# Kernel tuning notes

Hardware: AMD Instinct MI355X
Metric: run time of the kernel (lower is better)

Reference implementation:

```python
import jax, jax.numpy as jnp
import numpy as np

NEG_SLOPE_GAT = 0.2   # GATConv internal leaky_relu slope (PyG default)
NEG_SLOPE = 0.01      # nn.LeakyReLU default slope


def _gat(h_src_in, h_dst_in, src, dst, Wsrc, Wdst, a_s, a_d, b, n_dst, self_loops):
    """Single-head PyG-style GATConv: gather -> score -> edge softmax -> scatter-sum."""
    hs = h_src_in @ Wsrc            # [N_src, C]
    hd = h_dst_in @ Wdst            # [N_dst, C]
    if self_loops:                  # static flag; same node set on both sides
        loop = jnp.arange(n_dst, dtype=src.dtype)
        src = jnp.concatenate([src, loop])
        dst = jnp.concatenate([dst, loop])
    # attention logits per edge
    e = jax.nn.leaky_relu((hs @ a_s)[src] + (hd @ a_d)[dst], NEG_SLOPE_GAT)  # [E]
    # softmax over edges sharing a destination node
    m = jax.ops.segment_max(e, dst, num_segments=n_dst)
    ex = jnp.exp(e - m[dst])
    denom = jax.ops.segment_sum(ex, dst, num_segments=n_dst)
    alpha = ex / denom[dst]
    out = jax.ops.segment_sum(hs[src] * alpha[:, None], dst, num_segments=n_dst)
    return out + b


def setup_inputs() -> dict:
    key = jax.random.key(0)
    ks = iter(jax.random.split(key, 64))
    NB, NP = 100_000, 50_000
    E_bb, E_pp, E_bp = 800_000, 400_000, 400_000
    FB, FP, H, H2 = 32, 34, 64, 32
    rn = lambda shape, s=0.05: jax.random.normal(next(ks), shape, jnp.float32) * s
    d = {}
    d['x_b'] = rn((NB, FB), 1.0)
    d['x_p'] = rn((NP, FP), 1.0)
    d['ei_bb'] = jax.random.randint(next(ks), (2, E_bb), 0, NB, jnp.int32)
    d['ei_pp'] = jax.random.randint(next(ks), (2, E_pp), 0, NP, jnp.int32)
    d['ei_bp_src'] = jax.random.randint(next(ks), (E_bp,), 0, NB, jnp.int32)
    d['ei_bp_dst'] = jax.random.randint(next(ks), (E_bp,), 0, NP, jnp.int32)
    d['W_in_b'] = rn((FB, H)); d['b_in_b'] = jnp.zeros((H,), jnp.float32)
    d['W_in_p'] = rn((FP, H)); d['b_in_p'] = jnp.zeros((H,), jnp.float32)
    for tag, cin, cout in (('1', H, H), ('2', H, H2)):
        d['W_bb' + tag] = rn((cin, cout)); d['as_bb' + tag] = rn((cout,)); d['ad_bb' + tag] = rn((cout,)); d['b_bb' + tag] = jnp.zeros((cout,), jnp.float32)
        d['W_pp' + tag] = rn((cin, cout)); d['as_pp' + tag] = rn((cout,)); d['ad_pp' + tag] = rn((cout,)); d['b_pp' + tag] = jnp.zeros((cout,), jnp.float32)
        d['Ws_bp' + tag] = rn((cin, cout)); d['Wd_bp' + tag] = rn((cin, cout)); d['as_bp' + tag] = rn((cout,)); d['ad_bp' + tag] = rn((cout,)); d['b_bp' + tag] = jnp.zeros((cout,), jnp.float32)
    d['W_out'] = rn((H2, 1)); d['b_out'] = jnp.zeros((1,), jnp.float32)
    return d


def reference(x_b, x_p, ei_bb, ei_pp, ei_bp_src, ei_bp_dst,
              W_in_b, b_in_b, W_in_p, b_in_p,
              W_bb1, as_bb1, ad_bb1, b_bb1, W_pp1, as_pp1, ad_pp1, b_pp1,
              Ws_bp1, Wd_bp1, as_bp1, ad_bp1, b_bp1,
              W_bb2, as_bb2, ad_bb2, b_bb2, W_pp2, as_pp2, ad_pp2, b_pp2,
              Ws_bp2, Wd_bp2, as_bp2, ad_bp2, b_bp2,
              W_out, b_out):
    NB, NP = x_b.shape[0], x_p.shape[0]
    lr = lambda v: jax.nn.leaky_relu(v, NEG_SLOPE)
    # input projections (dropout is eval-mode identity)
    hb = lr(x_b @ W_in_b + b_in_b)
    hp = lr(x_p @ W_in_p + b_in_p)
    # hetero conv 1 (sum aggregation over relations sharing a dst type)
    ob = _gat(hb, hb, ei_bb[0], ei_bb[1], W_bb1, W_bb1, as_bb1, ad_bb1, b_bb1, NB, True)
    op = (_gat(hp, hp, ei_pp[0], ei_pp[1], W_pp1, W_pp1, as_pp1, ad_pp1, b_pp1, NP, True)
          + _gat(hb, hp, ei_bp_src, ei_bp_dst, Ws_bp1, Wd_bp1, as_bp1, ad_bp1, b_bp1, NP, False))
    hb, hp = lr(ob), lr(op)
    # hetero conv 2
    ob2 = _gat(hb, hb, ei_bb[0], ei_bb[1], W_bb2, W_bb2, as_bb2, ad_bb2, b_bb2, NB, True)
    op2 = (_gat(hp, hp, ei_pp[0], ei_pp[1], W_pp2, W_pp2, as_pp2, ad_pp2, b_pp2, NP, True)
           + _gat(hb, hp, ei_bp_src, ei_bp_dst, Ws_bp2, Wd_bp2, as_bp2, ad_bp2, b_bp2, NP, False))
    hp = lr(op2)
    return hp @ W_out + b_out  # [NP, 1]
```

## Files before the change

kernel.cpp:

```cpp
#include <hip/hip_runtime.h>
#include <hip/hip_bf16.h>
#include <cstdint>
#include <cstddef>


typedef __attribute__((ext_vector_type(8))) short short8;
typedef __attribute__((ext_vector_type(4))) float f32x4;
typedef unsigned int u32;

#define ABITS 9
#define CHUNKE 4096

static __device__ __forceinline__ float b2f(__hip_bfloat16 v) { return __bfloat162float(v); }

static __device__ __forceinline__ float ldf(const void* p, int i, int bf) {
    return bf ? __bfloat162float(((const __hip_bfloat16*)p)[i]) : ((const float*)p)[i];
}

static __device__ __forceinline__ short f2bs(float f) {
    __hip_bfloat16 h = __float2bfloat16(f);
    return *reinterpret_cast<short*>(&h);
}
static __device__ __forceinline__ float bs2f(short s) {
    __hip_bfloat16 h = *reinterpret_cast<__hip_bfloat16*>(&s);
    return __bfloat162float(h);
}
static __device__ __forceinline__ float lo16(u32 u) { return bs2f((short)(u & 0xffffu)); }
static __device__ __forceinline__ float hi16(u32 u) { return bs2f((short)(u >> 16)); }
static __device__ __forceinline__ u32 pack2(float x, float y) {
    return (u32)(unsigned short)f2bs(x) | ((u32)(unsigned short)f2bs(y) << 16);
}
static __device__ __forceinline__ float sel4(const float* a, int i) {
    return i == 0 ? a[0] : i == 1 ? a[1] : i == 2 ? a[2] : a[3];
}
static __device__ __forceinline__ float lrelu2(float x) { return x > 0.f ? x : 0.2f * x; }

__global__ __launch_bounds__(256) void k_detect(const unsigned* __restrict__ w,
                                                int* __restrict__ flag)
{
    __shared__ int s_cnt;
    if (threadIdx.x == 0) s_cnt = 0;
    __syncthreads();
    int c = 0;
#pragma unroll
    for (int j = 0; j < 4; ++j) {
        unsigned u = w[threadIdx.x * 4 + j];
        unsigned e = (u >> 7) & 0xffu;
        c += (e >= 100u && e <= 145u) ? 1 : 0;
    }
    atomicAdd(&s_cnt, c);
    __syncthreads();
    if (threadIdx.x == 0) *flag = (s_cnt > 614) ? 1 : 0;
}

__global__ __launch_bounds__(256) void k_bkt_hist(
    const int* __restrict__ bb_d, const int* __restrict__ pp_d,
    const int* __restrict__ bp_d, int* __restrict__ histM,
    int E_bb, int E_pp, int E_bp, int NB, int NP, int nbkt, int nblk)
{
    __shared__ int h[512];
    for (int i = threadIdx.x; i < nbkt; i += 256) h[i] = 0;
    __syncthreads();
    int E_all = E_bb + E_pp + E_bp;
    int base = blockIdx.x * CHUNKE;
    int end = base + CHUNKE < E_all ? base + CHUNKE : E_all;
    for (int i = base + threadIdx.x; i < end; i += 256) {
        int d;
        if (i < E_bb) d = bb_d[i];
        else if (i < E_bb + E_pp) d = NB + pp_d[i - E_bb];
        else d = NB + NP + bp_d[i - E_bb - E_pp];
        atomicAdd(&h[d >> ABITS], 1);
    }
    __syncthreads();
    for (int i = threadIdx.x; i < nbkt; i += 256)
        histM[(size_t)i * nblk + blockIdx.x] = h[i];
}

__global__ __launch_bounds__(1024) void k_scan1(const int* __restrict__ deg,
                                                int* __restrict__ out,
                                                int* __restrict__ bsum, int n)
{
    __shared__ int wsum[16];
    int gid = blockIdx.x * 1024 + threadIdx.x;
    int lane = threadIdx.x & 63, wid = threadIdx.x >> 6;
    int v = (gid < n) ? deg[gid] : 0;
    int x = v;
#pragma unroll
    for (int off = 1; off < 64; off <<= 1) {
        int y = __shfl_up(x, off, 64);
        if (lane >= off) x += y;
    }
    if (lane == 63) wsum[wid] = x;
    __syncthreads();
    if (wid == 0 && lane < 16) {
        int w0 = wsum[lane];
#pragma unroll
        for (int off = 1; off < 16; off <<= 1) {
            int y = __shfl_up(w0, off, 16);
            if (lane >= off) w0 += y;
        }
        wsum[lane] = w0;
    }
    __syncthreads();
    int base = (wid > 0) ? wsum[wid - 1] : 0;
    int incl = base + x;
    if (gid < n) out[gid] = incl - v;
    if (threadIdx.x == 1023) bsum[blockIdx.x] = incl;
}

__global__ __launch_bounds__(1024) void k_scan2(int* __restrict__ bsum, int nb)
{
    __shared__ int wsum[16];
    int lane = threadIdx.x & 63, wid = threadIdx.x >> 6;
    int v = (threadIdx.x < nb) ? bsum[threadIdx.x] : 0;
    int x = v;
#pragma unroll
    for (int off = 1; off < 64; off <<= 1) {
        int y = __shfl_up(x, off, 64);
        if (lane >= off) x += y;
    }
    if (lane == 63) wsum[wid] = x;
    __syncthreads();
    if (wid == 0 && lane < 16) {
        int w0 = wsum[lane];
#pragma unroll
        for (int off = 1; off < 16; off <<= 1) {
            int y = __shfl_up(w0, off, 16);
            if (lane >= off) w0 += y;
        }
        wsum[lane] = w0;
    }
    __syncthreads();
    int base = (wid > 0) ? wsum[wid - 1] : 0;
    if (threadIdx.x < nb) bsum[threadIdx.x] = base + x - v;
}

__global__ __launch_bounds__(1024) void k_scan3(int* __restrict__ indptr,
                                                const int* __restrict__ bsum,
                                                int n, int E)
{
    int gid = blockIdx.x * 1024 + threadIdx.x;
    if (gid < n) indptr[gid] += bsum[blockIdx.x];
    if (gid == 0) indptr[n] = E;
}

__global__ __launch_bounds__(256) void k_bkt_scatter(
    const int* __restrict__ bb_s, const int* __restrict__ bb_d,
    const int* __restrict__ pp_s, const int* __restrict__ pp_d,
    const int* __restrict__ bp_s, const int* __restrict__ bp_d,
    const int* __restrict__ histS, unsigned* __restrict__ ebuf,
    int E_bb, int E_pp, int E_bp, int NB, int NP, int nbkt, int nblk)
{
    __shared__ int cur[512];
    for (int i = threadIdx.x; i < nbkt; i += 256)
        cur[i] = histS[(size_t)i * nblk + blockIdx.x];
    __syncthreads();
    int E_all = E_bb + E_pp + E_bp;
    int base = blockIdx.x * CHUNKE;
    int end = base + CHUNKE < E_all ? base + CHUNKE : E_all;
    for (int i = base + threadIdx.x; i < end; i += 256) {
        int s, d;
        if (i < E_bb) { s = bb_s[i]; d = bb_d[i]; }
        else if (i < E_bb + E_pp) { int j = i - E_bb; s = pp_s[j]; d = NB + pp_d[j]; }
        else { int j = i - E_bb - E_pp; s = bp_s[j]; d = NB + NP + bp_d[j]; }
        int p = atomicAdd(&cur[d >> ABITS], 1);
        ebuf[p] = ((unsigned)(d & ((1 << ABITS) - 1)) << 20) | (unsigned)s;
    }
}

__global__ __launch_bounds__(256) void k_deg(
    const unsigned* __restrict__ ebuf, const int* __restrict__ histS,
    int* __restrict__ deg, int NALL, int E_all, int nbkt, int nblk)
{
    __shared__ int h[1 << ABITS];
    int b = blockIdx.x;
    int d0 = b << ABITS;
    int nloc = NALL - d0 < (1 << ABITS) ? NALL - d0 : (1 << ABITS);
    for (int i = threadIdx.x; i < nloc; i += 256) h[i] = 0;
    __syncthreads();
    int s0 = histS[(size_t)b * nblk];
    int s1 = histS[(size_t)(b + 1) * nblk];
    for (int i = s0 + threadIdx.x; i < s1; i += 256)
        atomicAdd(&h[ebuf[i] >> 20], 1);
    __syncthreads();
    for (int i = threadIdx.x; i < nloc; i += 256) deg[d0 + i] = h[i];
}

__global__ __launch_bounds__(256) void k_place(
    const unsigned* __restrict__ ebuf, const int* __restrict__ histS,
    const int* __restrict__ ip, int* __restrict__ sidx,
    int NALL, int E_all, int nbkt, int nblk)
{
    __shared__ int cur[1 << ABITS];
    int b = blockIdx.x;
    int d0 = b << ABITS;
    int nloc = NALL - d0 < (1 << ABITS) ? NALL - d0 : (1 << ABITS);
    for (int i = threadIdx.x; i < nloc; i += 256) cur[i] = ip[d0 + i];
    __syncthreads();
    int s0 = histS[(size_t)b * nblk];
    int s1 = histS[(size_t)(b + 1) * nblk];
    for (int i = s0 + threadIdx.x; i < s1; i += 256) {
        unsigned e = ebuf[i];
        int p = atomicAdd(&cur[e >> 20], 1);
        sidx[p] = (int)(e & 0xFFFFFu);
    }
}

template <int CIN>
__global__ __launch_bounds__(256) void k_in_proj_mfma(
    const void* __restrict__ X, const void* __restrict__ W, const void* __restrict__ B,
    __hip_bfloat16* __restrict__ Y, int M, const int* __restrict__ flag)
{
    const int bf = *flag;
    constexpr int KP = 40;
    __shared__ short WT[64 * KP];
    __shared__ float bl[64];
    for (int i = threadIdx.x; i < 64 * CIN; i += 256) {
        int n = i / CIN, k = i - n * CIN;
        WT[n * KP + k] = f2bs(ldf(W, k * 64 + n, bf));
    }
    if (threadIdx.x < 64) bl[threadIdx.x] = ldf(B, threadIdx.x, bf);
    __syncthreads();

    int lane = threadIdx.x & 63;
    int wv   = threadIdx.x >> 6;
    int m = lane & 15, quad = lane >> 4;
    int row0 = (blockIdx.x * 4 + wv) * 16;
    if (row0 >= M) return;

    int arow = row0 + m; if (arow >= M) arow = M - 1;
    short8 a;
#pragma unroll
    for (int j = 0; j < 8; ++j)
        a[j] = f2bs(ldf(X, arow * CIN + quad * 8 + j, bf));

    f32x4 acc[4] = {};
#pragma unroll
    for (int t = 0; t < 4; ++t) {
        short8 b = *(const short8*)&WT[((lane & 15) + 16 * t) * KP + quad * 8];
        acc[t] = __builtin_amdgcn_mfma_f32_16x16x32_bf16(a, b, acc[t], 0, 0, 0);
    }

    if (CIN == 34) {
        float x32[4], x33[4];
#pragma unroll
        for (int r = 0; r < 4; ++r) {
            int row = row0 + quad * 4 + r; if (row >= M) row = M - 1;
            x32[r] = ldf(X, row * CIN + 32, bf);
            x33[r] = ldf(X, row * CIN + 33, bf);
        }
#pragma unroll
        for (int t = 0; t < 4; ++t) {
            int col = (lane & 15) + 16 * t;
            float w32 = bs2f(WT[col * KP + 32]);
            float w33 = bs2f(WT[col * KP + 33]);
#pragma unroll
            for (int r = 0; r < 4; ++r)
                acc[t][r] += x32[r] * w32 + x33[r] * w33;
        }
    }

#pragma unroll
    for (int t = 0; t < 4; ++t) {
        int col = (lane & 15) + 16 * t;
        float bb = bl[col];
#pragma unroll
        for (int r = 0; r < 4; ++r) {
            int row = row0 + quad * 4 + r;
            if (row < M) {
                float v = acc[t][r] + bb;
                v = v > 0.f ? v : 0.01f * v;
                Y[(size_t)row * 64 + col] = __float2bfloat16(v);
            }
        }
    }
}

template <int N, bool STORE>
__global__ __launch_bounds__(256) void k_gat_proj_mfma(
    const __hip_bfloat16* __restrict__ H, const void* __restrict__ W,
    const void* __restrict__ a_s, const void* __restrict__ a_d,
    __hip_bfloat16* __restrict__ HS, float* __restrict__ SS, float* __restrict__ SD,
    int M, const int* __restrict__ flag)
{
    const int bf = *flag;
    constexpr int KP = 72;
    constexpr int T = N / 16;
    __shared__ short WT[N * KP];
    for (int i = threadIdx.x; i < N * 64; i += 256) {
        int n = i >> 6, k = i & 63;
        WT[n * KP + k] = f2bs(ldf(W, k * N + n, bf));
    }
    __syncthreads();

    int lane = threadIdx.x & 63;
    int wv   = threadIdx.x >> 6;
    int m = lane & 15, quad = lane >> 4;
    int row0 = (blockIdx.x * 4 + wv) * 16;
    if (row0 >= M) return;

    const short* Hs = (const short*)H;
    int arow = row0 + m; if (arow >= M) arow = M - 1;

    f32x4 acc[T] = {};
#pragma unroll
    for (int ks = 0; ks < 2; ++ks) {
        short8 a = *(const short8*)&Hs[(size_t)arow * 64 + ks * 32 + quad * 8];
#pragma unroll
        for (int t = 0; t < T; ++t) {
            short8 b = *(const short8*)&WT[((lane & 15) + 16 * t) * KP + ks * 32 + quad * 8];
            acc[t] = __builtin_amdgcn_mfma_f32_16x16x32_bf16(a, b, acc[t], 0, 0, 0);
        }
    }

    float asv[T], adv[T];
#pragma unroll
    for (int t = 0; t < T; ++t) {
        int col = (lane & 15) + 16 * t;
        asv[t] = ldf(a_s, col, bf);
        adv[t] = ldf(a_d, col, bf);
    }
    float vs[4] = {}, vd[4] = {};
#pragma unroll
    for (int t = 0; t < T; ++t)
#pragma unroll
        for (int r = 0; r < 4; ++r) {
            vs[r] += acc[t][r] * asv[t];
            vd[r] += acc[t][r] * adv[t];
        }
#pragma unroll
    for (int off = 1; off < 16; off <<= 1)
#pragma unroll
        for (int r = 0; r < 4; ++r) {
            vs[r] += __shfl_xor(vs[r], off);
            vd[r] += __shfl_xor(vd[r], off);
        }
    int c = lane & 15;
    if (c < 8) {
        int row = row0 + quad * 4 + (c & 3);
        if (row < M) {
            if (c < 4) SS[row] = sel4(vs, c & 3);
            else       SD[row] = sel4(vd, c & 3);
        }
    }

    if (STORE) {
#pragma unroll
        for (int t = 0; t < T; ++t) {
            int col = (lane & 15) + 16 * t;
#pragma unroll
            for (int r = 0; r < 4; ++r) {
                int row = row0 + quad * 4 + r;
                if (row < M)
                    HS[(size_t)row * N + col] = __float2bfloat16(acc[t][r]);
            }
        }
    }
}

template <int N1, int N2, bool S1, bool S2>
__global__ __launch_bounds__(256) void k_gat_proj_dual(
    const __hip_bfloat16* __restrict__ H,
    const void* __restrict__ W1, const void* __restrict__ W2,
    const void* __restrict__ as1, const void* __restrict__ ad1,
    const void* __restrict__ as2, const void* __restrict__ ad2,
    __hip_bfloat16* __restrict__ HS1, __hip_bfloat16* __restrict__ HS2,
    float* __restrict__ SS1, float* __restrict__ SD1,
    float* __restrict__ SS2, float* __restrict__ SD2,
    int M, const int* __restrict__ flag)
{
    const int bf = *flag;
    constexpr int KP = 72;
    constexpr int T1 = N1 / 16, T2 = N2 / 16, T = T1 + T2;
    __shared__ short WT[(N1 + N2) * KP];
    for (int i = threadIdx.x; i < N1 * 64; i += 256) {
        int n = i >> 6, k = i & 63;
        WT[n * KP + k] = f2bs(ldf(W1, k * N1 + n, bf));
    }
    for (int i = threadIdx.x; i < N2 * 64; i += 256) {
        int n = i >> 6, k = i & 63;
        WT[(N1 + n) * KP + k] = f2bs(ldf(W2, k * N2 + n, bf));
    }
    __syncthreads();

    int lane = threadIdx.x & 63;
    int wv   = threadIdx.x >> 6;
    int m = lane & 15, quad = lane >> 4;
    int row0 = (blockIdx.x * 4 + wv) * 16;
    if (row0 >= M) return;

    const short* Hs = (const short*)H;
    int arow = row0 + m; if (arow >= M) arow = M - 1;

    f32x4 acc[T] = {};
#pragma unroll
    for (int ks = 0; ks < 2; ++ks) {
        short8 a = *(const short8*)&Hs[(size_t)arow * 64 + ks * 32 + quad * 8];
#pragma unroll
        for (int t = 0; t < T; ++t) {
            short8 b = *(const short8*)&WT[((lane & 15) + 16 * t) * KP + ks * 32 + quad * 8];
            acc[t] = __builtin_amdgcn_mfma_f32_16x16x32_bf16(a, b, acc[t], 0, 0, 0);
        }
    }

    float vs1[4] = {}, vd1[4] = {}, vs2[4] = {}, vd2[4] = {};
#pragma unroll
    for (int t = 0; t < T1; ++t) {
        int col = (lane & 15) + 16 * t;
        float av = ldf(as1, col, bf), dv = ldf(ad1, col, bf);
#pragma unroll
        for (int r = 0; r < 4; ++r) {
            vs1[r] += acc[t][r] * av;
            vd1[r] += acc[t][r] * dv;
        }
    }
#pragma unroll
    for (int t = 0; t < T2; ++t) {
        int col = (lane & 15) + 16 * t;
        float av = ldf(as2, col, bf), dv = ldf(ad2, col, bf);
#pragma unroll
        for (int r = 0; r < 4; ++r) {
            vs2[r] += acc[T1 + t][r] * av;
            vd2[r] += acc[T1 + t][r] * dv;
        }
    }
#pragma unroll
    for (int off = 1; off < 16; off <<= 1)
#pragma unroll
        for (int r = 0; r < 4; ++r) {
            vs1[r] += __shfl_xor(vs1[r], off);
            vd1[r] += __shfl_xor(vd1[r], off);
            vs2[r] += __shfl_xor(vs2[r], off);
            vd2[r] += __shfl_xor(vd2[r], off);
        }
    int c = lane & 15;
    {
        int row = row0 + quad * 4 + (c & 3);
        if (row < M) {
            if (c < 4)       SS1[row] = sel4(vs1, c & 3);
            else if (c < 8)  SD1[row] = sel4(vd1, c & 3);
            else if (c < 12) SS2[row] = sel4(vs2, c & 3);
            else             SD2[row] = sel4(vd2, c & 3);
        }
    }

    if (S1) {
#pragma unroll
        for (int t = 0; t < T1; ++t) {
            int col = (lane & 15) + 16 * t;
#pragma unroll
            for (int r = 0; r < 4; ++r) {
                int row = row0 + quad * 4 + r;
                if (row < M)
                    HS1[(size_t)row * N1 + col] = __float2bfloat16(acc[t][r]);
            }
        }
    }
    if (S2) {
#pragma unroll
        for (int t = 0; t < T2; ++t) {
            int col = (lane & 15) + 16 * t;
#pragma unroll
            for (int r = 0; r < 4; ++r) {
                int row = row0 + quad * 4 + r;
                if (row < M)
                    HS2[(size_t)row * N2 + col] = __float2bfloat16(acc[T1 + t][r]);
            }
        }
    }
}

__global__ __launch_bounds__(256) void k_gather1(
    const int* __restrict__ ip, const int* __restrict__ si,
    const float* __restrict__ SS, const float* __restrict__ SD,
    const __hip_bfloat16* __restrict__ HS, const void* __restrict__ bias,
    __hip_bfloat16* __restrict__ OUT, int M, const int* __restrict__ flag)
{
    const int bf = *flag;
    int lane = threadIdx.x & 63;
    int half = lane >> 5, hl = lane & 31;
    int d = blockIdx.x * 4 + (threadIdx.x >> 6);
    if (d >= M) return;
    const u32* H32 = (const u32*)HS;
    float sdd = SD[d];
    float ax = 0.f, ay = 0.f, den = 0.f;
    if (half == 0) {
        float ex = __expf(lrelu2(SS[d] + sdd));
        u32 h = H32[(size_t)d * 32 + hl];
        ax = lo16(h) * ex; ay = hi16(h) * ex; den = ex;
    }
    int j1 = ip[d + 1];
    int j = ip[d] + half;
    for (; j + 2 < j1; j += 4) {
        int s0 = si[j], s1 = si[j + 2];
        u32 h0 = H32[(size_t)s0 * 32 + hl];
        u32 h1 = H32[(size_t)s1 * 32 + hl];
        float e0 = __expf(lrelu2(SS[s0] + sdd));
        float e1 = __expf(lrelu2(SS[s1] + sdd));
        ax += lo16(h0) * e0 + lo16(h1) * e1;
        ay += hi16(h0) * e0 + hi16(h1) * e1;
        den += e0 + e1;
    }
    if (j < j1) {
        int s0 = si[j];
        u32 h0 = H32[(size_t)s0 * 32 + hl];
        float e0 = __expf(lrelu2(SS[s0] + sdd));
        ax += lo16(h0) * e0; ay += hi16(h0) * e0; den += e0;
    }
    ax += __shfl_xor(ax, 32); ay += __shfl_xor(ay, 32); den += __shfl_xor(den, 32);
    if (half == 0) {
        float vx = ax / den + ldf(bias, 2 * hl, bf);
        float vy = ay / den + ldf(bias, 2 * hl + 1, bf);
        vx = vx > 0.f ? vx : 0.01f * vx;
        vy = vy > 0.f ? vy : 0.01f * vy;
        ((u32*)OUT)[(size_t)d * 32 + hl] = pack2(vx, vy);
    }
}

__global__ __launch_bounds__(256) void k_gather2(
    const int* __restrict__ ip1, const int* __restrict__ si,
    const float* __restrict__ SS1, const float* __restrict__ SD1,
    const __hip_bfloat16* __restrict__ HS1,
    const int* __restrict__ ip2,
    const float* __restrict__ SS2, const float* __restrict__ SD2,
    const __hip_bfloat16* __restrict__ HS2,
    const void* __restrict__ b1, const void* __restrict__ b2,
    __hip_bfloat16* __restrict__ OUT, int M, const int* __restrict__ flag)
{
    const int bf = *flag;
    int lane = threadIdx.x & 63;
    int half = lane >> 5, hl = lane & 31;
    int d = blockIdx.x * 4 + (threadIdx.x >> 6);
    if (d >= M) return;
    const u32* H1 = (const u32*)HS1;
    const u32* H2 = (const u32*)HS2;
    float sdd = SD1[d];
    float a1x = 0.f, a1y = 0.f, den1 = 0.f;
    if (half == 0) {
        float ex = __expf(lrelu2(SS1[d] + sdd));
        u32 h = H1[(size_t)d * 32 + hl];
        a1x = lo16(h) * ex; a1y = hi16(h) * ex; den1 = ex;
    }
    int j1 = ip1[d + 1];
    int j = ip1[d] + half;
    for (; j + 2 < j1; j += 4) {
        int s0 = si[j], s1 = si[j + 2];
        u32 h0 = H1[(size_t)s0 * 32 + hl];
        u32 h1 = H1[(size_t)s1 * 32 + hl];
        float e0 = __expf(lrelu2(SS1[s0] + sdd));
        float e1 = __expf(lrelu2(SS1[s1] + sdd));
        a1x += lo16(h0) * e0 + lo16(h1) * e1;
        a1y += hi16(h0) * e0 + hi16(h1) * e1;
        den1 += e0 + e1;
    }
    if (j < j1) {
        int s0 = si[j];
        u32 h0 = H1[(size_t)s0 * 32 + hl];
        float e0 = __expf(lrelu2(SS1[s0] + sdd));
        a1x += lo16(h0) * e0; a1y += hi16(h0) * e0; den1 += e0;
    }
    float sdd2 = SD2[d];
    float a2x = 0.f, a2y = 0.f, den2 = 0.f;
    j1 = ip2[d + 1];
    j = ip2[d] + half;
    for (; j + 2 < j1; j += 4) {
        int s0 = si[j], s1 = si[j + 2];
        u32 h0 = H2[(size_t)s0 * 32 + hl];
        u32 h1 = H2[(size_t)s1 * 32 + hl];
        float e0 = __expf(lrelu2(SS2[s0] + sdd2));
        float e1 = __expf(lrelu2(SS2[s1] + sdd2));
        a2x += lo16(h0) * e0 + lo16(h1) * e1;
        a2y += hi16(h0) * e0 + hi16(h1) * e1;
        den2 += e0 + e1;
    }
    if (j < j1) {
        int s0 = si[j];
        u32 h0 = H2[(size_t)s0 * 32 + hl];
        float e0 = __expf(lrelu2(SS2[s0] + sdd2));
        a2x += lo16(h0) * e0; a2y += hi16(h0) * e0; den2 += e0;
    }
    a1x += __shfl_xor(a1x, 32); a1y += __shfl_xor(a1y, 32); den1 += __shfl_xor(den1, 32);
    a2x += __shfl_xor(a2x, 32); a2y += __shfl_xor(a2y, 32); den2 += __shfl_xor(den2, 32);
    if (half == 0) {
        float inv2 = den2 > 0.f ? 1.f / den2 : 0.f;
        float vx = a1x / den1 + a2x * inv2 + ldf(b1, 2 * hl, bf) + ldf(b2, 2 * hl, bf);
        float vy = a1y / den1 + a2y * inv2 + ldf(b1, 2 * hl + 1, bf) + ldf(b2, 2 * hl + 1, bf);
        vx = vx > 0.f ? vx : 0.01f * vx;
        vy = vy > 0.f ? vy : 0.01f * vy;
        ((u32*)OUT)[(size_t)d * 32 + hl] = pack2(vx, vy);
    }
}

__global__ __launch_bounds__(256) void k_gather_out(
    const int* __restrict__ ip1, const int* __restrict__ si,
    const float* __restrict__ SS1, const float* __restrict__ SD1,
    const __hip_bfloat16* __restrict__ HS1,
    const int* __restrict__ ip2,
    const float* __restrict__ SS2, const float* __restrict__ SD2,
    const __hip_bfloat16* __restrict__ HS2,
    const void* __restrict__ b1, const void* __restrict__ b2,
    const void* __restrict__ Wout, const void* __restrict__ bout,
    void* __restrict__ OUT, int M, const int* __restrict__ flag)
{
    const int bf = *flag;
    int lane = threadIdx.x & 63;
    int q = lane >> 4, hl = lane & 15;
    int d = blockIdx.x * 4 + (threadIdx.x >> 6);
    if (d >= M) return;
    const u32* H1 = (const u32*)HS1;
    const u32* H2 = (const u32*)HS2;
    float sdd = SD1[d];
    float a1x = 0.f, a1y = 0.f, den1 = 0.f;
    if (q == 0) {
        float ex = __expf(lrelu2(SS1[d] + sdd));
        u32 h = H1[(size_t)d * 16 + hl];
        a1x = lo16(h) * ex; a1y = hi16(h) * ex; den1 = ex;
    }
    int j1 = ip1[d + 1];
    for (int j = ip1[d] + q; j < j1; j += 4) {
        int s0 = si[j];
        u32 h0 = H1[(size_t)s0 * 16 + hl];
        float e0 = __expf(lrelu2(SS1[s0] + sdd));
        a1x += lo16(h0) * e0; a1y += hi16(h0) * e0; den1 += e0;
    }
    float sdd2 = SD2[d];
    float a2x = 0.f, a2y = 0.f, den2 = 0.f;
    j1 = ip2[d + 1];
    for (int j = ip2[d] + q; j < j1; j += 4) {
        int s0 = si[j];
        u32 h0 = H2[(size_t)s0 * 16 + hl];
        float e0 = __expf(lrelu2(SS2[s0] + sdd2));
        a2x += lo16(h0) * e0; a2y += hi16(h0) * e0; den2 += e0;
    }
    a1x += __shfl_xor(a1x, 16); a1y += __shfl_xor(a1y, 16); den1 += __shfl_xor(den1, 16);
    a2x += __shfl_xor(a2x, 16); a2y += __shfl_xor(a2y, 16); den2 += __shfl_xor(den2, 16);
    a1x += __shfl_xor(a1x, 32); a1y += __shfl_xor(a1y, 32); den1 += __shfl_xor(den1, 32);
    a2x += __shfl_xor(a2x, 32); a2y += __shfl_xor(a2y, 32); den2 += __shfl_xor(den2, 32);
    float inv2 = den2 > 0.f ? 1.f / den2 : 0.f;
    float vx = a1x / den1 + a2x * inv2 + ldf(b1, 2 * hl, bf) + ldf(b2, 2 * hl, bf);
    float vy = a1y / den1 + a2y * inv2 + ldf(b1, 2 * hl + 1, bf) + ldf(b2, 2 * hl + 1, bf);
    vx = vx > 0.f ? vx : 0.01f * vx;
    vy = vy > 0.f ? vy : 0.01f * vy;
    float t = vx * ldf(Wout, 2 * hl, bf) + vy * ldf(Wout, 2 * hl + 1, bf);
#pragma unroll
    for (int off = 1; off < 16; off <<= 1) t += __shfl_xor(t, off);
    if (lane == 0) {
        float r = t + ldf(bout, 0, bf);
        if (bf) ((__hip_bfloat16*)OUT)[d] = __float2bfloat16(r);
        else    ((float*)OUT)[d] = r;
    }
}

extern "C" void kernel_launch(void* const* d_in, const int* in_sizes, int n_in,
                              void* d_out, int out_size, void* d_ws, size_t ws_size,
                              hipStream_t stream)
{
    const void* x_b = d_in[0];
    const void* x_p = d_in[1];
    const int* ei_bb = (const int*)d_in[2];
    const int* ei_pp = (const int*)d_in[3];
    const int* bp_s  = (const int*)d_in[4];
    const int* bp_d  = (const int*)d_in[5];
    const void *W_in_b = d_in[6],  *b_in_b = d_in[7];
    const void *W_in_p = d_in[8],  *b_in_p = d_in[9];
    const void *W_bb1 = d_in[10], *as_bb1 = d_in[11], *ad_bb1 = d_in[12], *b_bb1 = d_in[13];
    const void *W_pp1 = d_in[14], *as_pp1 = d_in[15], *ad_pp1 = d_in[16], *b_pp1 = d_in[17];
    const void *Ws_bp1 = d_in[18], *Wd_bp1 = d_in[19], *as_bp1 = d_in[20], *ad_bp1 = d_in[21], *b_bp1 = d_in[22];
    const void *W_pp2 = d_in[27], *as_pp2 = d_in[28], *ad_pp2 = d_in[29], *b_pp2 = d_in[30];
    const void *Ws_bp2 = d_in[31], *Wd_bp2 = d_in[32], *as_bp2 = d_in[33], *ad_bp2 = d_in[34], *b_bp2 = d_in[35];
    const void *W_out = d_in[36], *b_out = d_in[37];

    const int NB   = in_sizes[0] / 32;
    const int NP   = in_sizes[1] / 34;
    const int E_bb = in_sizes[2] / 2;
    const int E_pp = in_sizes[3] / 2;
    const int E_bp = in_sizes[4];
    const int E_all = E_bb + E_pp + E_bp;
    const int NALL  = NB + 2 * NP;
    const int* bb_s = ei_bb;  const int* bb_d = ei_bb + E_bb;
    const int* pp_s = ei_pp;  const int* pp_d = ei_pp + E_pp;
    (void)ws_size; (void)n_in; (void)out_size;

    const int nbkt  = (NALL + (1 << ABITS) - 1) >> ABITS;
    const int nblk  = (E_all + CHUNKE - 1) / CHUNKE;
    const int nh    = nbkt * nblk;

    typedef __hip_bfloat16 bf16;
    char* base = (char*)d_ws;
    size_t o = 0;
    auto alloc = [&](size_t bytes) { char* p = base + o; o += (bytes + 255) & ~(size_t)255; return p; };

    int* flag  = (int*)alloc(256);
    int* bsum  = (int*)alloc(1024 * 4);
    int* histM = (int*)alloc((size_t)nh * 4);
    int* histS = (int*)alloc((size_t)(nh + 1) * 4);
    int* degA  = (int*)alloc((size_t)NALL * 4);
    int* ip_all = (int*)alloc((size_t)(NALL + 1) * 4);
    unsigned* ebuf = (unsigned*)alloc((size_t)E_all * 4);
    int* si_all = (int*)alloc((size_t)E_all * 4);
    float* ss_bb = (float*)alloc((size_t)NB * 4);
    float* sd_bb = (float*)alloc((size_t)NB * 4);
    float* ss_bp = (float*)alloc((size_t)NB * 4);
    float* ss_pp = (float*)alloc((size_t)NP * 4);
    float* sd_pp = (float*)alloc((size_t)NP * 4);
    float* sd_bp = (float*)alloc((size_t)NP * 4);
    float* ss2_bp = ss_bb;
    float* ss2_pp = ss_pp;
    float* sd2_pp = sd_pp;
    float* sd2_bp = sd_bp;
    float* junkNB = (float*)degA;
    float* junkNP = (float*)(degA + NB);

    char* S1 = alloc((size_t)NB * 64 * 2);
    char* S2 = alloc((size_t)NP * 64 * 2);
    char* S3 = alloc((size_t)NB * 64 * 2);
    char* S4 = alloc((size_t)NB * 64 * 2);
    char* S5 = alloc((size_t)NB * 64 * 2);
    char* S6 = alloc((size_t)NP * 64 * 2);

    bf16* hb     = (bf16*)S1;
    bf16* hp     = (bf16*)S2;
    bf16* hs_bb  = (bf16*)S3;
    bf16* hb2    = (bf16*)S4;
    bf16* hs_bp  = (bf16*)S5;
    bf16* hs_pp  = (bf16*)S6;
    bf16* hp2    = (bf16*)S3;
    bf16* hs2_pp = (bf16*)S2;
    bf16* hs2_bp = (bf16*)S1;

    auto cdiv = [](int a, int b) { return (a + b - 1) / b; };

    k_detect<<<1, 256, 0, stream>>>((const unsigned*)x_b, flag);

    k_bkt_hist<<<nblk, 256, 0, stream>>>(bb_d, pp_d, bp_d, histM,
                                         E_bb, E_pp, E_bp, NB, NP, nbkt, nblk);
    int sb1 = cdiv(nh, 1024);
    k_scan1<<<sb1, 1024, 0, stream>>>(histM, histS, bsum, nh);
    k_scan2<<<1, 1024, 0, stream>>>(bsum, sb1);
    k_scan3<<<sb1, 1024, 0, stream>>>(histS, bsum, nh, E_all);
    k_bkt_scatter<<<nblk, 256, 0, stream>>>(bb_s, bb_d, pp_s, pp_d, bp_s, bp_d,
                                            histS, ebuf, E_bb, E_pp, E_bp, NB, NP, nbkt, nblk);
    k_deg<<<nbkt, 256, 0, stream>>>(ebuf, histS, degA, NALL, E_all, nbkt, nblk);
    int sb2 = cdiv(NALL, 1024);
    k_scan1<<<sb2, 1024, 0, stream>>>(degA, ip_all, bsum, NALL);
    k_scan2<<<1, 1024, 0, stream>>>(bsum, sb2);
    k_scan3<<<sb2, 1024, 0, stream>>>(ip_all, bsum, NALL, E_all);
    k_place<<<nbkt, 256, 0, stream>>>(ebuf, histS, ip_all, si_all, NALL, E_all, nbkt, nblk);

    const int* ip_bb = ip_all;
    const int* ip_pp = ip_all + NB;
    const int* ip_bp = ip_all + NB + NP;

    k_in_proj_mfma<32><<<cdiv(NB, 64), 256, 0, stream>>>(x_b, W_in_b, b_in_b, hb, NB, flag);
    k_in_proj_mfma<34><<<cdiv(NP, 64), 256, 0, stream>>>(x_p, W_in_p, b_in_p, hp, NP, flag);

    k_gat_proj_dual<64, 64, true, true><<<cdiv(NB, 64), 256, 0, stream>>>(
        hb, W_bb1, Ws_bp1, as_bb1, ad_bb1, as_bp1, ad_bp1,
        hs_bb, hs_bp, ss_bb, sd_bb, ss_bp, junkNB, NB, flag);
    k_gather1<<<cdiv(NB, 4), 256, 0, stream>>>(ip_bb, si_all, ss_bb, sd_bb, hs_bb, b_bb1, hb2, NB, flag);

    k_gat_proj_dual<64, 64, true, false><<<cdiv(NP, 64), 256, 0, stream>>>(
        hp, W_pp1, Wd_bp1, as_pp1, ad_pp1, as_bp1, ad_bp1,
        hs_pp, nullptr, ss_pp, sd_pp, junkNP, sd_bp, NP, flag);
    k_gather2<<<cdiv(NP, 4), 256, 0, stream>>>(ip_pp, si_all, ss_pp, sd_pp, hs_pp,
                                               ip_bp, ss_bp, sd_bp, hs_bp,
                                               b_pp1, b_bp1, hp2, NP, flag);

    k_gat_proj_dual<32, 32, true, false><<<cdiv(NP, 64), 256, 0, stream>>>(
        hp2, W_pp2, Wd_bp2, as_pp2, ad_pp2, as_bp2, ad_bp2,
        hs2_pp, nullptr, ss2_pp, sd2_pp, junkNP, sd2_bp, NP, flag);
    k_gat_proj_mfma<32, true><<<cdiv(NB, 64), 256, 0, stream>>>(
        hb2, Ws_bp2, as_bp2, ad_bp2, hs2_bp, ss2_bp, junkNB, NB, flag);

    k_gather_out<<<cdiv(NP, 4), 256, 0, stream>>>(ip_pp, si_all, ss2_pp, sd2_pp, hs2_pp,
                                                  ip_bp, ss2_bp, sd2_bp, hs2_bp,
                                                  b_pp2, b_bp2, W_out, b_out, d_out, NP, flag);
}
```

Measured before the change: 434.1 us.

## Merge CSR build passes and fuse paired projection/gather launches

Folds the dtype detection into the histogram kernel. Replaces the degree count, three-pass scan and placement kernels with one per-bucket finalize kernel that does a local scan using the bucket offsets. Merges the B/P input projections, the layer-1 projections, the layer-1 gathers and the layer-2 projections into single launches that dispatch on block index. The aim is to cut kernel launch and serialization overhead; buffers are re-aliased to free the degree array.

```diff
diff --git a/kernel.cpp b/kernel.cpp
--- a/kernel.cpp
+++ b/kernel.cpp
@@ -7,22 +7,23 @@
 typedef __attribute__((ext_vector_type(8))) short short8;
 typedef __attribute__((ext_vector_type(4))) float f32x4;
 typedef unsigned int u32;
+typedef __hip_bfloat16 bf16;
 
 #define ABITS 9
 #define CHUNKE 4096
 
-static __device__ __forceinline__ float b2f(__hip_bfloat16 v) { return __bfloat162float(v); }
+static __device__ __forceinline__ float b2f(bf16 v) { return __bfloat162float(v); }
 
 static __device__ __forceinline__ float ldf(const void* p, int i, int bf) {
-    return bf ? __bfloat162float(((const __hip_bfloat16*)p)[i]) : ((const float*)p)[i];
+    return bf ? __bfloat162float(((const bf16*)p)[i]) : ((const float*)p)[i];
 }
 
 static __device__ __forceinline__ short f2bs(float f) {
-    __hip_bfloat16 h = __float2bfloat16(f);
+    bf16 h = __float2bfloat16(f);
     return *reinterpret_cast<short*>(&h);
 }
 static __device__ __forceinline__ float bs2f(short s) {
-    __hip_bfloat16 h = *reinterpret_cast<__hip_bfloat16*>(&s);
+    bf16 h = *reinterpret_cast<bf16*>(&s);
     return __bfloat162float(h);
 }
 static __device__ __forceinline__ float lo16(u32 u) { return bs2f((short)(u & 0xffffu)); }
@@ -35,30 +36,28 @@
 }
 static __device__ __forceinline__ float lrelu2(float x) { return x > 0.f ? x : 0.2f * x; }
 
-__global__ __launch_bounds__(256) void k_detect(const unsigned* __restrict__ w,
-                                                int* __restrict__ flag)
-{
-    __shared__ int s_cnt;
-    if (threadIdx.x == 0) s_cnt = 0;
-    __syncthreads();
-    int c = 0;
-#pragma unroll
-    for (int j = 0; j < 4; ++j) {
-        unsigned u = w[threadIdx.x * 4 + j];
-        unsigned e = (u >> 7) & 0xffu;
-        c += (e >= 100u && e <= 145u) ? 1 : 0;
-    }
-    atomicAdd(&s_cnt, c);
-    __syncthreads();
-    if (threadIdx.x == 0) *flag = (s_cnt > 614) ? 1 : 0;
-}
-
 __global__ __launch_bounds__(256) void k_bkt_hist(
     const int* __restrict__ bb_d, const int* __restrict__ pp_d,
     const int* __restrict__ bp_d, int* __restrict__ histM,
+    const unsigned* __restrict__ probe_w, int* __restrict__ flag,
     int E_bb, int E_pp, int E_bp, int NB, int NP, int nbkt, int nblk)
 {
-    __shared__ int h[512];
+    if (blockIdx.x == 0) {
+        __shared__ int s_cnt;
+        if (threadIdx.x == 0) s_cnt = 0;
+        __syncthreads();
+        int c = 0;
+#pragma unroll
+        for (int j = 0; j < 4; ++j) {
+            unsigned u = probe_w[threadIdx.x * 4 + j];
+            unsigned e = (u >> 7) & 0xffu;
+            c += (e >= 100u && e <= 145u) ? 1 : 0;
+        }
+        atomicAdd(&s_cnt, c);
+        __syncthreads();
+        if (threadIdx.x == 0) *flag = (s_cnt > 614) ? 1 : 0;
+    }
+    __shared__ int h[1 << ABITS];
     for (int i = threadIdx.x; i < nbkt; i += 256) h[i] = 0;
     __syncthreads();
     int E_all = E_bb + E_pp + E_bp;
@@ -151,7 +150,7 @@
     const int* __restrict__ histS, unsigned* __restrict__ ebuf,
     int E_bb, int E_pp, int E_bp, int NB, int NP, int nbkt, int nblk)
 {
-    __shared__ int cur[512];
+    __shared__ int cur[1 << ABITS];
     for (int i = threadIdx.x; i < nbkt; i += 256)
         cur[i] = histS[(size_t)i * nblk + blockIdx.x];
     __syncthreads();
@@ -168,53 +167,64 @@
     }
 }
 
-__global__ __launch_bounds__(256) void k_deg(
+__global__ __launch_bounds__(256) void k_finalize(
     const unsigned* __restrict__ ebuf, const int* __restrict__ histS,
-    int* __restrict__ deg, int NALL, int E_all, int nbkt, int nblk)
+    int* __restrict__ ip_all, int* __restrict__ sidx,
+    int NALL, int E_all, int nbkt, int nblk)
 {
     __shared__ int h[1 << ABITS];
+    __shared__ int pre[1 << ABITS];
+    __shared__ int wq[4];
     int b = blockIdx.x;
     int d0 = b << ABITS;
     int nloc = NALL - d0 < (1 << ABITS) ? NALL - d0 : (1 << ABITS);
-    for (int i = threadIdx.x; i < nloc; i += 256) h[i] = 0;
+    int t = threadIdx.x;
+    for (int i = t; i < (1 << ABITS); i += 256) h[i] = 0;
     __syncthreads();
     int s0 = histS[(size_t)b * nblk];
     int s1 = histS[(size_t)(b + 1) * nblk];
-    for (int i = s0 + threadIdx.x; i < s1; i += 256)
+    for (int i = s0 + t; i < s1; i += 256)
         atomicAdd(&h[ebuf[i] >> 20], 1);
     __syncthreads();
-    for (int i = threadIdx.x; i < nloc; i += 256) deg[d0 + i] = h[i];
-}
-
-__global__ __launch_bounds__(256) void k_place(
-    const unsigned* __restrict__ ebuf, const int* __restrict__ histS,
-    const int* __restrict__ ip, int* __restrict__ sidx,
-    int NALL, int E_all, int nbkt, int nblk)
-{
-    __shared__ int cur[1 << ABITS];
-    int b = blockIdx.x;
-    int d0 = b << ABITS;
-    int nloc = NALL - d0 < (1 << ABITS) ? NALL - d0 : (1 << ABITS);
-    for (int i = threadIdx.x; i < nloc; i += 256) cur[i] = ip[d0 + i];
-    __syncthreads();
-    int s0 = histS[(size_t)b * nblk];
-    int s1 = histS[(size_t)(b + 1) * nblk];
-    for (int i = s0 + threadIdx.x; i < s1; i += 256) {
+    int v0 = h[2 * t], v1 = h[2 * t + 1];
+    int ps = v0 + v1;
+    int lane = t & 63, wid = t >> 6;
+    int x = ps;
+#pragma unroll
+    for (int off = 1; off < 64; off <<= 1) {
+        int y = __shfl_up(x, off, 64);
+        if (lane >= off) x += y;
+    }
+    if (lane == 63) wq[wid] = x;
+    __syncthreads();
+    if (t == 0) {
+        int a = 0;
+#pragma unroll
+        for (int w = 0; w < 4; ++w) { int tmp = wq[w]; wq[w] = a; a += tmp; }
+    }
+    __syncthreads();
+    int excl = wq[wid] + x - ps;
+    pre[2 * t]     = excl;
+    pre[2 * t + 1] = excl + v0;
+    __syncthreads();
+    for (int i = t; i < nloc; i += 256) ip_all[d0 + i] = s0 + pre[i];
+    if (d0 + nloc == NALL && t == 0) ip_all[NALL] = E_all;
+    for (int i = t; i < (1 << ABITS); i += 256) h[i] = s0 + pre[i];
+    __syncthreads();
+    for (int i = s0 + t; i < s1; i += 256) {
         unsigned e = ebuf[i];
-        int p = atomicAdd(&cur[e >> 20], 1);
+        int p = atomicAdd(&h[e >> 20], 1);
         sidx[p] = (int)(e & 0xFFFFFu);
     }
 }
 
 template <int CIN>
-__global__ __launch_bounds__(256) void k_in_proj_mfma(
+static __device__ __forceinline__ void in_proj_body(
+    short* WT, float* bl, int bid,
     const void* __restrict__ X, const void* __restrict__ W, const void* __restrict__ B,
-    __hip_bfloat16* __restrict__ Y, int M, const int* __restrict__ flag)
-{
-    const int bf = *flag;
+    bf16* __restrict__ Y, int M, int bf)
+{
     constexpr int KP = 40;
-    __shared__ short WT[64 * KP];
-    __shared__ float bl[64];
     for (int i = threadIdx.x; i < 64 * CIN; i += 256) {
         int n = i / CIN, k = i - n * CIN;
         WT[n * KP + k] = f2bs(ldf(W, k * 64 + n, bf));
@@ -225,7 +235,7 @@
     int lane = threadIdx.x & 63;
     int wv   = threadIdx.x >> 6;
     int m = lane & 15, quad = lane >> 4;
-    int row0 = (blockIdx.x * 4 + wv) * 16;
+    int row0 = (bid * 4 + wv) * 16;
     if (row0 >= M) return;
 
     int arow = row0 + m; if (arow >= M) arow = M - 1;
@@ -236,9 +246,9 @@
 
     f32x4 acc[4] = {};
 #pragma unroll
-    for (int t = 0; t < 4; ++t) {
-        short8 b = *(const short8*)&WT[((lane & 15) + 16 * t) * KP + quad * 8];
-        acc[t] = __builtin_amdgcn_mfma_f32_16x16x32_bf16(a, b, acc[t], 0, 0, 0);
+    for (int tt = 0; tt < 4; ++tt) {
+        short8 bfr = *(const short8*)&WT[((lane & 15) + 16 * tt) * KP + quad * 8];
+        acc[tt] = __builtin_amdgcn_mfma_f32_16x16x32_bf16(a, bfr, acc[tt], 0, 0, 0);
     }
 
     if (CIN == 34) {
@@ -250,25 +260,25 @@
             x33[r] = ldf(X, row * CIN + 33, bf);
         }
 #pragma unroll
-        for (int t = 0; t < 4; ++t) {
-            int col = (lane & 15) + 16 * t;
+        for (int tt = 0; tt < 4; ++tt) {
+            int col = (lane & 15) + 16 * tt;
             float w32 = bs2f(WT[col * KP + 32]);
             float w33 = bs2f(WT[col * KP + 33]);
 #pragma unroll
             for (int r = 0; r < 4; ++r)
-                acc[t][r] += x32[r] * w32 + x33[r] * w33;
-        }
-    }
-
-#pragma unroll
-    for (int t = 0; t < 4; ++t) {
-        int col = (lane & 15) + 16 * t;
+                acc[tt][r] += x32[r] * w32 + x33[r] * w33;
+        }
+    }
+
+#pragma unroll
+    for (int tt = 0; tt < 4; ++tt) {
+        int col = (lane & 15) + 16 * tt;
         float bb = bl[col];
 #pragma unroll
         for (int r = 0; r < 4; ++r) {
             int row = row0 + quad * 4 + r;
             if (row < M) {
-                float v = acc[t][r] + bb;
+                float v = acc[tt][r] + bb;
                 v = v > 0.f ? v : 0.01f * v;
                 Y[(size_t)row * 64 + col] = __float2bfloat16(v);
             }
@@ -276,27 +286,47 @@
     }
 }
 
-template <int N, bool STORE>
-__global__ __launch_bounds__(256) void k_gat_proj_mfma(
-    const __hip_bfloat16* __restrict__ H, const void* __restrict__ W,
-    const void* __restrict__ a_s, const void* __restrict__ a_d,
-    __hip_bfloat16* __restrict__ HS, float* __restrict__ SS, float* __restrict__ SD,
-    int M, const int* __restrict__ flag)
+__global__ __launch_bounds__(256) void k_in_proj_all(
+    const void* __restrict__ Xb, const void* __restrict__ Wb, const void* __restrict__ Bb,
+    bf16* __restrict__ Yb, int MB,
+    const void* __restrict__ Xp, const void* __restrict__ Wp, const void* __restrict__ Bp,
+    bf16* __restrict__ Yp, int MP, const int* __restrict__ flag)
 {
     const int bf = *flag;
+    __shared__ short WT[64 * 40];
+    __shared__ float bl[64];
+    int nbb = (MB + 63) >> 6;
+    if (blockIdx.x < nbb) in_proj_body<32>(WT, bl, blockIdx.x, Xb, Wb, Bb, Yb, MB, bf);
+    else                  in_proj_body<34>(WT, bl, blockIdx.x - nbb, Xp, Wp, Bp, Yp, MP, bf);
+}
+
+template <int N1, int N2, bool S1F, bool S2F>
+static __device__ __forceinline__ void dual_body(
+    short* WT, int bid, const bf16* __restrict__ H,
+    const void* __restrict__ W1, const void* __restrict__ W2,
+    const void* __restrict__ as1, const void* __restrict__ ad1,
+    const void* __restrict__ as2, const void* __restrict__ ad2,
+    bf16* __restrict__ HS1, bf16* __restrict__ HS2,
+    float* __restrict__ SS1, float* __restrict__ SD1,
+    float* __restrict__ SS2, float* __restrict__ SD2,
+    int M, int bf)
+{
     constexpr int KP = 72;
-    constexpr int T = N / 16;
-    __shared__ short WT[N * KP];
-    for (int i = threadIdx.x; i < N * 64; i += 256) {
+    constexpr int T1 = N1 / 16, T2 = N2 / 16, T = T1 + T2;
+    for (int i = threadIdx.x; i < N1 * 64; i += 256) {
         int n = i >> 6, k = i & 63;
-        WT[n * KP + k] = f2bs(ldf(W, k * N + n, bf));
+        WT[n * KP + k] = f2bs(ldf(W1, k * N1 + n, bf));
+    }
+    for (int i = threadIdx.x; i < N2 * 64; i += 256) {
+        int n = i >> 6, k = i & 63;
+        WT[(N1 + n) * KP + k] = f2bs(ldf(W2, k * N2 + n, bf));
     }
     __syncthreads();
 
     int lane = threadIdx.x & 63;
     int wv   = threadIdx.x >> 6;
     int m = lane & 15, quad = lane >> 4;
-    int row0 = (blockIdx.x * 4 + wv) * 16;
+    int row0 = (bid * 4 + wv) * 16;
     if (row0 >= M) return;
 
     const short* Hs = (const short*)H;
@@ -307,121 +337,31 @@
     for (int ks = 0; ks < 2; ++ks) {
         short8 a = *(const short8*)&Hs[(size_t)arow * 64 + ks * 32 + quad * 8];
 #pragma unroll
-        for (int t = 0; t < T; ++t) {
-            short8 b = *(const short8*)&WT[((lane & 15) + 16 * t) * KP + ks * 32 + quad * 8];
-            acc[t] = __builtin_amdgcn_mfma_f32_16x16x32_bf16(a, b, acc[t], 0, 0, 0);
-        }
-    }
-
-    float asv[T], adv[T];
-#pragma unroll
-    for (int t = 0; t < T; ++t) {
-        int col = (lane & 15) + 16 * t;
-        asv[t] = ldf(a_s, col, bf);
-        adv[t] = ldf(a_d, col, bf);
-    }
-    float vs[4] = {}, vd[4] = {};
-#pragma unroll
-    for (int t = 0; t < T; ++t)
+        for (int tt = 0; tt < T; ++tt) {
+            short8 bfr = *(const short8*)&WT[((lane & 15) + 16 * tt) * KP + ks * 32 + quad * 8];
+            acc[tt] = __builtin_amdgcn_mfma_f32_16x16x32_bf16(a, bfr, acc[tt], 0, 0, 0);
+        }
+    }
+
+    float vs1[4] = {}, vd1[4] = {}, vs2[4] = {}, vd2[4] = {};
+#pragma unroll
+    for (int tt = 0; tt < T1; ++tt) {
+        int col = (lane & 15) + 16 * tt;
+        float av = ldf(as1, col, bf), dv = ldf(ad1, col, bf);
 #pragma unroll
         for (int r = 0; r < 4; ++r) {
-            vs[r] += acc[t][r] * asv[t];
-            vd[r] += acc[t][r] * adv[t];
-        }
-#pragma unroll
-    for (int off = 1; off < 16; off <<= 1)
+            vs1[r] += acc[tt][r] * av;
+            vd1[r] += acc[tt][r] * dv;
+        }
+    }
+#pragma unroll
+    for (int tt = 0; tt < T2; ++tt) {
+        int col = (lane & 15) + 16 * tt;
+        float av = ldf(as2, col, bf), dv = ldf(ad2, col, bf);
 #pragma unroll
         for (int r = 0; r < 4; ++r) {
-            vs[r] += __shfl_xor(vs[r], off);
-            vd[r] += __shfl_xor(vd[r], off);
-        }
-    int c = lane & 15;
-    if (c < 8) {
-        int row = row0 + quad * 4 + (c & 3);
-        if (row < M) {
-            if (c < 4) SS[row] = sel4(vs, c & 3);
-            else       SD[row] = sel4(vd, c & 3);
-        }
-    }
-
-    if (STORE) {
-#pragma unroll
-        for (int t = 0; t < T; ++t) {
-            int col = (lane & 15) + 16 * t;
-#pragma unroll
-            for (int r = 0; r < 4; ++r) {
-                int row = row0 + quad * 4 + r;
-                if (row < M)
-                    HS[(size_t)row * N + col] = __float2bfloat16(acc[t][r]);
-            }
-        }
-    }
-}
-
-template <int N1, int N2, bool S1, bool S2>
-__global__ __launch_bounds__(256) void k_gat_proj_dual(
-    const __hip_bfloat16* __restrict__ H,
-    const void* __restrict__ W1, const void* __restrict__ W2,
-    const void* __restrict__ as1, const void* __restrict__ ad1,
-    const void* __restrict__ as2, const void* __restrict__ ad2,
-    __hip_bfloat16* __restrict__ HS1, __hip_bfloat16* __restrict__ HS2,
-    float* __restrict__ SS1, float* __restrict__ SD1,
-    float* __restrict__ SS2, float* __restrict__ SD2,
-    int M, const int* __restrict__ flag)
-{
-    const int bf = *flag;
-    constexpr int KP = 72;
-    constexpr int T1 = N1 / 16, T2 = N2 / 16, T = T1 + T2;
-    __shared__ short WT[(N1 + N2) * KP];
-    for (int i = threadIdx.x; i < N1 * 64; i += 256) {
-        int n = i >> 6, k = i & 63;
-        WT[n * KP + k] = f2bs(ldf(W1, k * N1 + n, bf));
-    }
-    for (int i = threadIdx.x; i < N2 * 64; i += 256) {
-        int n = i >> 6, k = i & 63;
-        WT[(N1 + n) * KP + k] = f2bs(ldf(W2, k * N2 + n, bf));
-    }
-    __syncthreads();
-
-    int lane = threadIdx.x & 63;
-    int wv   = threadIdx.x >> 6;
-    int m = lane & 15, quad = lane >> 4;
-    int row0 = (blockIdx.x * 4 + wv) * 16;
-    if (row0 >= M) return;
-
-    const short* Hs = (const short*)H;
-    int arow = row0 + m; if (arow >= M) arow = M - 1;
-
-    f32x4 acc[T] = {};
-#pragma unroll
-    for (int ks = 0; ks < 2; ++ks) {
-        short8 a = *(const short8*)&Hs[(size_t)arow * 64 + ks * 32 + quad * 8];
-#pragma unroll
-        for (int t = 0; t < T; ++t) {
-            short8 b = *(const short8*)&WT[((lane & 15) + 16 * t) * KP + ks * 32 + quad * 8];
-            acc[t] = __builtin_amdgcn_mfma_f32_16x16x32_bf16(a, b, acc[t], 0, 0, 0);
-        }
-    }
-
-    float vs1[4] = {}, vd1[4] = {}, vs2[4] = {}, vd2[4] = {};
-#pragma unroll
-    for (int t = 0; t < T1; ++t) {
-        int col = (lane & 15) + 16 * t;
-        float av = ldf(as1, col, bf), dv = ldf(ad1, col, bf);
-#pragma unroll
-        for (int r = 0; r < 4; ++r) {
-            vs1[r] += acc[t][r] * av;
-            vd1[r] += acc[t][r] * dv;
-        }
-    }
-#pragma unroll
-    for (int t = 0; t < T2; ++t) {
-        int col = (lane & 15) + 16 * t;
-        float av = ldf(as2, col, bf), dv = ldf(ad2, col, bf);
-#pragma unroll
-        for (int r = 0; r < 4; ++r) {
-            vs2[r] += acc[T1 + t][r] * av;
-            vd2[r] += acc[T1 + t][r] * dv;
+            vs2[r] += acc[T1 + tt][r] * av;
+            vd2[r] += acc[T1 + tt][r] * dv;
         }
     }
 #pragma unroll
@@ -444,42 +384,167 @@
         }
     }
 
-    if (S1) {
-#pragma unroll
-        for (int t = 0; t < T1; ++t) {
-            int col = (lane & 15) + 16 * t;
+    if (S1F) {
+#pragma unroll
+        for (int tt = 0; tt < T1; ++tt) {
+            int col = (lane & 15) + 16 * tt;
 #pragma unroll
             for (int r = 0; r < 4; ++r) {
                 int row = row0 + quad * 4 + r;
                 if (row < M)
-                    HS1[(size_t)row * N1 + col] = __float2bfloat16(acc[t][r]);
+                    HS1[(size_t)row * N1 + col] = __float2bfloat16(acc[tt][r]);
             }
         }
     }
-    if (S2) {
-#pragma unroll
-        for (int t = 0; t < T2; ++t) {
-            int col = (lane & 15) + 16 * t;
+    if (S2F) {
+#pragma unroll
+        for (int tt = 0; tt < T2; ++tt) {
+            int col = (lane & 15) + 16 * tt;
 #pragma unroll
             for (int r = 0; r < 4; ++r) {
                 int row = row0 + quad * 4 + r;
                 if (row < M)
-                    HS2[(size_t)row * N2 + col] = __float2bfloat16(acc[T1 + t][r]);
+                    HS2[(size_t)row * N2 + col] = __float2bfloat16(acc[T1 + tt][r]);
             }
         }
     }
 }
 
-__global__ __launch_bounds__(256) void k_gather1(
-    const int* __restrict__ ip, const int* __restrict__ si,
+template <int N, bool STORE>
+static __device__ __forceinline__ void proj_body(
+    short* WT, int bid, const bf16* __restrict__ H, const void* __restrict__ W,
+    const void* __restrict__ a_s, const void* __restrict__ a_d,
+    bf16* __restrict__ HS, float* __restrict__ SS, float* __restrict__ SD,
+    int M, int bf)
+{
+    constexpr int KP = 72;
+    constexpr int T = N / 16;
+    for (int i = threadIdx.x; i < N * 64; i += 256) {
+        int n = i >> 6, k = i & 63;
+        WT[n * KP + k] = f2bs(ldf(W, k * N + n, bf));
+    }
+    __syncthreads();
+
+    int lane = threadIdx.x & 63;
+    int wv   = threadIdx.x >> 6;
+    int m = lane & 15, quad = lane >> 4;
+    int row0 = (bid * 4 + wv) * 16;
+    if (row0 >= M) return;
+
+    const short* Hs = (const short*)H;
+    int arow = row0 + m; if (arow >= M) arow = M - 1;
+
+    f32x4 acc[T] = {};
+#pragma unroll
+    for (int ks = 0; ks < 2; ++ks) {
+        short8 a = *(const short8*)&Hs[(size_t)arow * 64 + ks * 32 + quad * 8];
+#pragma unroll
+        for (int tt = 0; tt < T; ++tt) {
+            short8 bfr = *(const short8*)&WT[((lane & 15) + 16 * tt) * KP + ks * 32 + quad * 8];
+            acc[tt] = __builtin_amdgcn_mfma_f32_16x16x32_bf16(a, bfr, acc[tt], 0, 0, 0);
+        }
+    }
+
+    float asv[T], adv[T];
+#pragma unroll
+    for (int tt = 0; tt < T; ++tt) {
+        int col = (lane & 15) + 16 * tt;
+        asv[tt] = ldf(a_s, col, bf);
+        adv[tt] = ldf(a_d, col, bf);
+    }
+    float vs[4] = {}, vd[4] = {};
+#pragma unroll
+    for (int tt = 0; tt < T; ++tt)
+#pragma unroll
+        for (int r = 0; r < 4; ++r) {
+            vs[r] += acc[tt][r] * asv[tt];
+            vd[r] += acc[tt][r] * adv[tt];
+        }
+#pragma unroll
+    for (int off = 1; off < 16; off <<= 1)
+#pragma unroll
+        for (int r = 0; r < 4; ++r) {
+            vs[r] += __shfl_xor(vs[r], off);
+            vd[r] += __shfl_xor(vd[r], off);
+        }
+    int c = lane & 15;
+    if (c < 8) {
+        int row = row0 + quad * 4 + (c & 3);
+        if (row < M) {
+            if (c < 4) SS[row] = sel4(vs, c & 3);
+            else       SD[row] = sel4(vd, c & 3);
+        }
+    }
+
+    if (STORE) {
+#pragma unroll
+        for (int tt = 0; tt < T; ++tt) {
+            int col = (lane & 15) + 16 * tt;
+#pragma unroll
+            for (int r = 0; r < 4; ++r) {
+                int row = row0 + quad * 4 + r;
+                if (row < M)
+                    HS[(size_t)row * N + col] = __float2bfloat16(acc[tt][r]);
+            }
+        }
+    }
+}
+
+__global__ __launch_bounds__(256) void k_dual64_all(
+    const bf16* __restrict__ hb,
+    const void* W_bb1, const void* Ws_bp1,
+    const void* as_bb1, const void* ad_bb1, const void* as_bp1, const void* ad_bp1,
+    bf16* hs_bb, bf16* hs_bp,
+    float* ss_bb, float* sd_bb, float* ss_bp, float* junkNB, int MB,
+    const bf16* __restrict__ hp,
+    const void* W_pp1, const void* Wd_bp1,
+    const void* as_pp1, const void* ad_pp1,
+    bf16* hs_pp, float* ss_pp, float* sd_pp, float* junkNP, float* sd_bp, int MP,
+    const int* __restrict__ flag)
+{
+    const int bf = *flag;
+    __shared__ short WT[128 * 72];
+    int nbb = (MB + 63) >> 6;
+    if (blockIdx.x < nbb)
+        dual_body<64, 64, true, true>(WT, blockIdx.x, hb, W_bb1, Ws_bp1,
+            as_bb1, ad_bb1, as_bp1, ad_bp1, hs_bb, hs_bp,
+            ss_bb, sd_bb, ss_bp, junkNB, MB, bf);
+    else
+        dual_body<64, 64, true, false>(WT, blockIdx.x - nbb, hp, W_pp1, Wd_bp1,
+            as_pp1, ad_pp1, as_bp1, ad_bp1, hs_pp, nullptr,
+            ss_pp, sd_pp, junkNP, sd_bp, MP, bf);
+}
+
+__global__ __launch_bounds__(256) void k_proj2_all(
+    const bf16* __restrict__ hp2,
+    const void* W_pp2, const void* Wd_bp2,
+    const void* as_pp2, const void* ad_pp2, const void* as_bp2, const void* ad_bp2,
+    bf16* hs2_pp, float* ss2_pp, float* sd2_pp, float* junkNP, float* sd2_bp, int MP,
+    const bf16* __restrict__ hb2,
+    const void* Ws_bp2, bf16* hs2_bp, float* ss2_bp, float* junkNB, int MB,
+    const int* __restrict__ flag)
+{
+    const int bf = *flag;
+    __shared__ short WT[64 * 72];
+    int npb = (MP + 63) >> 6;
+    if (blockIdx.x < npb)
+        dual_body<32, 32, true, false>(WT, blockIdx.x, hp2, W_pp2, Wd_bp2,
+            as_pp2, ad_pp2, as_bp2, ad_bp2, hs2_pp, nullptr,
+            ss2_pp, sd2_pp, junkNP, sd2_bp, MP, bf);
+    else
+        proj_body<32, true>(WT, blockIdx.x - npb, hb2, Ws_bp2,
+            as_bp2, ad_bp2, hs2_bp, ss2_bp, junkNB, MB, bf);
+}
+
+static __device__ __forceinline__ void gather1_body(
+    int bid, const int* __restrict__ ip, const int* __restrict__ si,
     const float* __restrict__ SS, const float* __restrict__ SD,
-    const __hip_bfloat16* __restrict__ HS, const void* __restrict__ bias,
-    __hip_bfloat16* __restrict__ OUT, int M, const int* __restrict__ flag)
-{
-    const int bf = *flag;
+    const bf16* __restrict__ HS, const void* __restrict__ bias,
+    bf16* __restrict__ OUT, int M, int bf)
+{
     int lane = threadIdx.x & 63;
     int half = lane >> 5, hl = lane & 31;
-    int d = blockIdx.x * 4 + (threadIdx.x >> 6);
+    int d = bid * 4 + (threadIdx.x >> 6);
     if (d >= M) return;
     const u32* H32 = (const u32*)HS;
     float sdd = SD[d];
@@ -517,20 +582,19 @@
     }
 }
 
-__global__ __launch_bounds__(256) void k_gather2(
-    const int* __restrict__ ip1, const int* __restrict__ si,
+static __device__ __forceinline__ void gather2_body(
+    int bid, const int* __restrict__ ip1, const int* __restrict__ si,
     const float* __restrict__ SS1, const float* __restrict__ SD1,
-    const __hip_bfloat16* __restrict__ HS1,
+    const bf16* __restrict__ HS1,
     const int* __restrict__ ip2,
     const float* __restrict__ SS2, const float* __restrict__ SD2,
-    const __hip_bfloat16* __restrict__ HS2,
+    const bf16* __restrict__ HS2,
     const void* __restrict__ b1, const void* __restrict__ b2,
-    __hip_bfloat16* __restrict__ OUT, int M, const int* __restrict__ flag)
-{
-    const int bf = *flag;
+    bf16* __restrict__ OUT, int M, int bf)
+{
     int lane = threadIdx.x & 63;
     int half = lane >> 5, hl = lane & 31;
-    int d = blockIdx.x * 4 + (threadIdx.x >> 6);
+    int d = bid * 4 + (threadIdx.x >> 6);
     if (d >= M) return;
     const u32* H1 = (const u32*)HS1;
     const u32* H2 = (const u32*)HS2;
@@ -591,13 +655,36 @@
     }
 }
 
+__global__ __launch_bounds__(256) void k_gather12(
+    const int* __restrict__ ip_bb, const int* __restrict__ si,
+    const float* __restrict__ ss_bb, const float* __restrict__ sd_bb,
+    const bf16* __restrict__ hs_bb, const void* __restrict__ b_bb1,
+    bf16* __restrict__ hb2, int NB,
+    const int* __restrict__ ip_pp, const int* __restrict__ ip_bp,
+    const float* __restrict__ ss_pp, const float* __restrict__ sd_pp,
+    const bf16* __restrict__ hs_pp,
+    const float* __restrict__ ss_bp, const float* __restrict__ sd_bp,
+    const bf16* __restrict__ hs_bp,
+    const void* __restrict__ b_pp1, const void* __restrict__ b_bp1,
+    bf16* __restrict__ hp2, int NP,
+    const int* __restrict__ flag)
+{
+    const int bf = *flag;
+    int nbb = (NB + 3) >> 2;
+    if (blockIdx.x < nbb)
+        gather1_body(blockIdx.x, ip_bb, si, ss_bb, sd_bb, hs_bb, b_bb1, hb2, NB, bf);
+    else
+        gather2_body(blockIdx.x - nbb, ip_pp, si, ss_pp, sd_pp, hs_pp,
+                     ip_bp, ss_bp, sd_bp, hs_bp, b_pp1, b_bp1, hp2, NP, bf);
+}
+
 __global__ __launch_bounds__(256) void k_gather_out(
     const int* __restrict__ ip1, const int* __restrict__ si,
     const float* __restrict__ SS1, const float* __restrict__ SD1,
-    const __hip_bfloat16* __restrict__ HS1,
+    const bf16* __restrict__ HS1,
     const int* __restrict__ ip2,
     const float* __restrict__ SS2, const float* __restrict__ SD2,
-    const __hip_bfloat16* __restrict__ HS2,
+    const bf16* __restrict__ HS2,
     const void* __restrict__ b1, const void* __restrict__ b2,
     const void* __restrict__ Wout, const void* __restrict__ bout,
     void* __restrict__ OUT, int M, const int* __restrict__ flag)
@@ -646,7 +733,7 @@
     for (int off = 1; off < 16; off <<= 1) t += __shfl_xor(t, off);
     if (lane == 0) {
         float r = t + ldf(bout, 0, bf);
-        if (bf) ((__hip_bfloat16*)OUT)[d] = __float2bfloat16(r);
+        if (bf) ((bf16*)OUT)[d] = __float2bfloat16(r);
         else    ((float*)OUT)[d] = r;
     }
 }
@@ -685,7 +772,6 @@
     const int nblk  = (E_all + CHUNKE - 1) / CHUNKE;
     const int nh    = nbkt * nblk;
 
-    typedef __hip_bfloat16 bf16;
     char* base = (char*)d_ws;
     size_t o = 0;
     auto alloc = [&](size_t bytes) { char* p = base + o; o += (bytes + 255) & ~(size_t)255; return p; };
@@ -694,7 +780,6 @@
     int* bsum  = (int*)alloc(1024 * 4);
     int* histM = (int*)alloc((size_t)nh * 4);
     int* histS = (int*)alloc((size_t)(nh + 1) * 4);
-    int* degA  = (int*)alloc((size_t)NALL * 4);
     int* ip_all = (int*)alloc((size_t)(NALL + 1) * 4);
     unsigned* ebuf = (unsigned*)alloc((size_t)E_all * 4);
     int* si_all = (int*)alloc((size_t)E_all * 4);
@@ -708,8 +793,8 @@
     float* ss2_pp = ss_pp;
     float* sd2_pp = sd_pp;
     float* sd2_bp = sd_bp;
-    float* junkNB = (float*)degA;
-    float* junkNP = (float*)(degA + NB);
+    float* junkNB = (float*)ebuf;
+    float* junkNP = (float*)ebuf + NB;
 
     char* S1 = alloc((size_t)NB * 64 * 2);
     char* S2 = alloc((size_t)NP * 64 * 2);
@@ -724,15 +809,14 @@
     bf16* hb2    = (bf16*)S4;
     bf16* hs_bp  = (bf16*)S5;
     bf16* hs_pp  = (bf16*)S6;
-    bf16* hp2    = (bf16*)S3;
-    bf16* hs2_pp = (bf16*)S2;
+    bf16* hp2    = (bf16*)S2;
+    bf16* hs2_pp = (bf16*)S3;
     bf16* hs2_bp = (bf16*)S1;
 
     auto cdiv = [](int a, int b) { return (a + b - 1) / b; };
 
-    k_detect<<<1, 256, 0, stream>>>((const unsigned*)x_b, flag);
-
     k_bkt_hist<<<nblk, 256, 0, stream>>>(bb_d, pp_d, bp_d, histM,
+                                         (const unsigned*)x_b, flag,
                                          E_bb, E_pp, E_bp, NB, NP, nbkt, nblk);
     int sb1 = cdiv(nh, 1024);
     k_scan1<<<sb1, 1024, 0, stream>>>(histM, histS, bsum, nh);
@@ -740,39 +824,33 @@
     k_scan3<<<sb1, 1024, 0, stream>>>(histS, bsum, nh, E_all);
     k_bkt_scatter<<<nblk, 256, 0, stream>>>(bb_s, bb_d, pp_s, pp_d, bp_s, bp_d,
                                             histS, ebuf, E_bb, E_pp, E_bp, NB, NP, nbkt, nblk);
-    k_deg<<<nbkt, 256, 0, stream>>>(ebuf, histS, degA, NALL, E_all, nbkt, nblk);
-    int sb2 = cdiv(NALL, 1024);
-    k_scan1<<<sb2, 1024, 0, stream>>>(degA, ip_all, bsum, NALL);
-    k_scan2<<<1, 1024, 0, stream>>>(bsum, sb2);
-    k_scan3<<<sb2, 1024, 0, stream>>>(ip_all, bsum, NALL, E_all);
-    k_place<<<nbkt, 256, 0, stream>>>(ebuf, histS, ip_all, si_all, NALL, E_all, nbkt, nblk);
+    k_finalize<<<nbkt, 256, 0, stream>>>(ebuf, histS, ip_all, si_all, NALL, E_all, nbkt, nblk);
 
     const int* ip_bb = ip_all;
     const int* ip_pp = ip_all + NB;
     const int* ip_bp = ip_all + NB + NP;
 
-    k_in_proj_mfma<32><<<cdiv(NB, 64), 256, 0, stream>>>(x_b, W_in_b, b_in_b, hb, NB, flag);
-    k_in_proj_mfma<34><<<cdiv(NP, 64), 256, 0, stream>>>(x_p, W_in_p, b_in_p, hp, NP, flag);
-
-    k_gat_proj_dual<64, 64, true, true><<<cdiv(NB, 64), 256, 0, stream>>>(
+    k_in_proj_all<<<cdiv(NB, 64) + cdiv(NP, 64), 256, 0, stream>>>(
+        x_b, W_in_b, b_in_b, hb, NB, x_p, W_in_p, b_in_p, hp, NP, flag);
+
+    k_dual64_all<<<cdiv(NB, 64) + cdiv(NP, 64), 256, 0, stream>>>(
         hb, W_bb1, Ws_bp1, as_bb1, ad_bb1, as_bp1, ad_bp1,
-        hs_bb, hs_bp, ss_bb, sd_bb, ss_bp, junkNB, NB, flag);
-    k_gather1<<<cdiv(NB, 4), 256, 0, stream>>>(ip_bb, si_all, ss_bb, sd_bb, hs_bb, b_bb1, hb2, NB, flag);
-
-    k_gat_proj_dual<64, 64, true, false><<<cdiv(NP, 64), 256, 0, stream>>>(
-        hp, W_pp1, Wd_bp1, as_pp1, ad_pp1, as_bp1, ad_bp1,
-        hs_pp, nullptr, ss_pp, sd_pp, junkNP, sd_bp, NP, flag);
-    k_gather2<<<cdiv(NP, 4), 256, 0, stream>>>(ip_pp, si_all, ss_pp, sd_pp, hs_pp,
-                                               ip_bp, ss_bp, sd_bp, hs_bp,
-                                               b_pp1, b_bp1, hp2, NP, flag);
-
-    k_gat_proj_dual<32, 32, true, false><<<cdiv(NP, 64), 256, 0, stream>>>(
+        hs_bb, hs_bp, ss_bb, sd_bb, ss_bp, junkNB, NB,
+        hp, W_pp1, Wd_bp1, as_pp1, ad_pp1,
+        hs_pp, ss_pp, sd_pp, junkNP, sd_bp, NP, flag);
+
+    k_gather12<<<cdiv(NB, 4) + cdiv(NP, 4), 256, 0, stream>>>(
+        ip_bb, si_all, ss_bb, sd_bb, hs_bb, b_bb1, hb2, NB,
+        ip_pp, ip_bp, ss_pp, sd_pp, hs_pp, ss_bp, sd_bp, hs_bp,
+        b_pp1, b_bp1, hp2, NP, flag);
+
+    k_proj2_all<<<cdiv(NP, 64) + cdiv(NB, 64), 256, 0, stream>>>(
         hp2, W_pp2, Wd_bp2, as_pp2, ad_pp2, as_bp2, ad_bp2,
-        hs2_pp, nullptr, ss2_pp, sd2_pp, junkNP, sd2_bp, NP, flag);
-    k_gat_proj_mfma<32, true><<<cdiv(NB, 64), 256, 0, stream>>>(
-        hb2, Ws_bp2, as_bp2, ad_bp2, hs2_bp, ss2_bp, junkNB, NB, flag);
-
-    k_gather_out<<<cdiv(NP, 4), 256, 0, stream>>>(ip_pp, si_all, ss2_pp, sd2_pp, hs2_pp,
-                                                  ip_bp, ss2_bp, sd2_bp, hs2_bp,
-                                                  b_pp2, b_bp2, W_out, b_out, d_out, NP, flag);
-}
+        hs2_pp, ss2_pp, sd2_pp, junkNP, sd2_bp, NP,
+        hb2, Ws_bp2, hs2_bp, ss2_bp, junkNB, NB, flag);
+
+    k_gather_out<<<cdiv(NP, 4), 256, 0, stream>>>(
+        ip_pp, si_all, ss2_pp, sd2_pp, hs2_pp,
+        ip_bp, ss2_bp, sd2_bp, hs2_bp,
+        b_pp2, b_bp2, W_out, b_out, d_out, NP, flag);
+}
```

Result: faster. 407.9 us (-6.0%).
